# Kernel tuning notes

Measured on AMD Instinct MI355X. Metric: run time of the kernel, lower is better.

## Reference

```python
import jax, jax.numpy as jnp
import numpy as np

D_MODEL = 1024
NUM_HEADS = 16
HEAD_DIM = D_MODEL // NUM_HEADS


def setup_inputs() -> dict:
    key = jax.random.key(0)
    ks = jax.random.split(key, 9)
    B, S = 2, 2048
    s = 1.0 / np.sqrt(D_MODEL)
    return {
        "x": jax.random.normal(ks[0], (B, S, D_MODEL), dtype=jnp.float32),
        "Wq": jax.random.normal(ks[1], (D_MODEL, D_MODEL), dtype=jnp.float32) * s,
        "bq": jnp.zeros((D_MODEL,), dtype=jnp.float32),
        "Wk": jax.random.normal(ks[2], (D_MODEL, D_MODEL), dtype=jnp.float32) * s,
        "bk": jnp.zeros((D_MODEL,), dtype=jnp.float32),
        "Wv": jax.random.normal(ks[3], (D_MODEL, D_MODEL), dtype=jnp.float32) * s,
        "bv": jnp.zeros((D_MODEL,), dtype=jnp.float32),
        "Wo": jax.random.normal(ks[4], (D_MODEL, D_MODEL), dtype=jnp.float32) * s,
        "bo": jnp.zeros((D_MODEL,), dtype=jnp.float32),
    }


def reference(x, Wq, bq, Wk, bk, Wv, bv, Wo, bo):
    B, S, _ = x.shape
    # projections; weights stored as (in, out) so y = x @ W + b
    def heads(y):  # [B,S,D] -> [B,H,S,Dh]
        return y.reshape(B, S, NUM_HEADS, HEAD_DIM).transpose(0, 2, 1, 3)

    Q = heads(x @ Wq + bq)
    K = heads(x @ Wk + bk)
    V = heads(x @ Wv + bv)
    scale = 1.0 / np.sqrt(HEAD_DIM).astype(np.float32)
    scores = jnp.einsum("bhqd,bhkd->bhqk", Q, K) * scale  # [B,H,S,S]
    attn = jax.nn.softmax(scores, axis=-1)
    ctx = jnp.einsum("bhqk,bhkd->bhqd", attn, V)  # [B,H,S,Dh]
    ctx = ctx.transpose(0, 2, 1, 3).reshape(B, S, D_MODEL)
    return ctx @ Wo + bo
```

## Files before the change

### kernel.cpp

```cpp
#include <hip/hip_runtime.h>
#include <hip/hip_bf16.h>

#define SEQ   2048
#define NH    16
#define HD    64
#define DM    1024
#define MROWS 4096

#define QSCALE 0.125f
#define RTHR 5.545177444479562f

typedef __attribute__((ext_vector_type(4))) float f32x4;
typedef __attribute__((ext_vector_type(8))) short s16x8;
typedef __attribute__((ext_vector_type(4))) short s16x4;

__device__ __forceinline__ short f2bf(float f) {
  union { float f; unsigned u; } v; v.f = f;
  return (short)((v.u + 0x7fff + ((v.u >> 16) & 1)) >> 16);
}

__device__ __forceinline__ void gload_lds16(const short* g, short* l) {
  __builtin_amdgcn_global_load_lds(
      (const __attribute__((address_space(1))) void*)g,
      (__attribute__((address_space(3))) void*)l, 16, 0, 0);
}

#define SWZ(row, gg) ((((row) << 3) + (((gg) ^ ((row) & 7)))) << 3)

__global__ void cvt_x(const float* __restrict__ x, short* __restrict__ xb) {
  int i = (blockIdx.x * 256 + threadIdx.x) * 8;
  const float4* p = reinterpret_cast<const float4*>(x + i);
  float4 a = p[0], b = p[1];
  s16x8 o;
  o[0] = f2bf(a.x); o[1] = f2bf(a.y); o[2] = f2bf(a.z); o[3] = f2bf(a.w);
  o[4] = f2bf(b.x); o[5] = f2bf(b.y); o[6] = f2bf(b.z); o[7] = f2bf(b.w);
  *reinterpret_cast<s16x8*>(xb + i) = o;
}

__global__ void wtrans(const float* __restrict__ Wq, const float* __restrict__ Wk,
                       const float* __restrict__ Wv, const float* __restrict__ Wo,
                       short* __restrict__ WT) {
  __shared__ float tile[64][65];
  const float* W = (blockIdx.z == 0) ? Wq : (blockIdx.z == 1) ? Wk : (blockIdx.z == 2) ? Wv : Wo;
  short* dst = WT + (size_t)blockIdx.z * DM * DM;
  int kbase = blockIdx.x * 64;
  int nbase = blockIdx.y * 64;
  int t = threadIdx.x;
  {
    int n4 = (t & 15) * 4;
    #pragma unroll
    for (int rr = 0; rr < 4; ++rr) {
      int r = (t >> 4) + 16 * rr;
      float4 v = *reinterpret_cast<const float4*>(W + (size_t)(kbase + r) * DM + nbase + n4);
      tile[r][n4] = v.x; tile[r][n4 + 1] = v.y; tile[r][n4 + 2] = v.z; tile[r][n4 + 3] = v.w;
    }
  }
  __syncthreads();
  {
    int n = t >> 2, kc = (t & 3) * 16;
    short tmp[16];
    #pragma unroll
    for (int j = 0; j < 16; ++j) tmp[j] = f2bf(tile[kc + j][n]);
    s16x8* q = reinterpret_cast<s16x8*>(dst + (size_t)(nbase + n) * DM + kbase + kc);
    q[0] = *reinterpret_cast<s16x8*>(tmp);
    q[1] = *reinterpret_cast<s16x8*>(tmp + 8);
  }
}

__global__ __launch_bounds__(256, 2) void gemm_qkv(
    const short* __restrict__ A, const short* __restrict__ BT,
    const float* __restrict__ bias0, const float* __restrict__ bias1,
    const float* __restrict__ bias2,
    short* __restrict__ oQ, short* __restrict__ oK, short* __restrict__ oVt) {
  __shared__ __align__(16) short As[128 * 64];
  __shared__ __align__(16) short Bs[128 * 64];
  const int lin = blockIdx.x;
  const int wg = (lin & 7) * 96 + (lin >> 3);
  const int bx = wg & 31;
  const int by = wg >> 5;
  const int lane = threadIdx.x & 63;
  const int wid = threadIdx.x >> 6;
  const int q15 = lane & 15, g4 = lane >> 4;
  const int mbase = bx * 128;
  const int nbase = by * 128;
  const int wm = wid >> 1, wn = wid & 1;

  f32x4 acc[4][4] = {};
  const int srow = lane >> 3;
  const int sg = (lane & 7) ^ srow;

  for (int k0 = 0; k0 < DM; k0 += 64) {
    #pragma unroll
    for (int j = 0; j < 4; ++j) {
      int c = wid * 4 + j;
      int row = c * 8 + srow;
      gload_lds16(A + (size_t)(mbase + row) * DM + k0 + sg * 8, As + c * 512);
      gload_lds16(BT + (size_t)(nbase + row) * DM + k0 + sg * 8, Bs + c * 512);
    }
    __syncthreads();
    #pragma unroll
    for (int ks = 0; ks < 2; ++ks) {
      s16x8 af[4], bfr[4];
      #pragma unroll
      for (int m = 0; m < 4; ++m)
        af[m] = *reinterpret_cast<const s16x8*>(As + SWZ(wm * 64 + m * 16 + q15, ks * 4 + g4));
      #pragma unroll
      for (int n = 0; n < 4; ++n)
        bfr[n] = *reinterpret_cast<const s16x8*>(Bs + SWZ(wn * 64 + n * 16 + q15, ks * 4 + g4));
      #pragma unroll
      for (int m = 0; m < 4; ++m)
        #pragma unroll
        for (int n = 0; n < 4; ++n)
          acc[m][n] = __builtin_amdgcn_mfma_f32_16x16x32_bf16(af[m], bfr[n], acc[m][n], 0, 0, 0);
    }
    __syncthreads();
  }

  const int r0 = mbase + wm * 64;
  const int c0 = nbase + wn * 64;
  #pragma unroll
  for (int m = 0; m < 4; ++m) {
    #pragma unroll
    for (int n = 0; n < 4; ++n) {
      int rr = r0 + m * 16 + g4 * 4;
      int cc = c0 + n * 16 + q15;
      int seg = cc >> 10, c1 = cc & 1023;
      const float* bp = (seg == 0) ? bias0 : (seg == 1) ? bias1 : bias2;
      float bv = bp[c1];
      int h = c1 >> 6, d = c1 & 63;
      if (seg == 2) {
        s16x4 o;
        #pragma unroll
        for (int i = 0; i < 4; ++i) o[i] = f2bf(acc[m][n][i] + bv);
        int b = rr >> 11, s = rr & 2047;
        *reinterpret_cast<s16x4*>(
            oVt + ((size_t)(b * NH + h) * HD + d) * SEQ + s) = o;
      } else {
        short* dst = (seg == 0) ? oQ : oK;
        #pragma unroll
        for (int i = 0; i < 4; ++i) {
          int r = rr + i;
          float v = acc[m][n][i] + bv;
          if (seg == 0) v *= QSCALE;
          int b = r >> 11, s = r & 2047;
          size_t idx = (((size_t)(b * NH + h) * SEQ + s) << 6) + d;
          dst[idx] = f2bf(v);
        }
      }
    }
  }
}

__global__ __launch_bounds__(256, 2) void gemm_o(
    const short* __restrict__ A, const short* __restrict__ BT,
    const float* __restrict__ bias, float* __restrict__ oF) {
  __shared__ __align__(16) short As[64 * 64];
  __shared__ __align__(16) short Bs[128 * 64];
  const int lin = blockIdx.x;
  const int wg = (lin & 7) * 64 + (lin >> 3);
  const int bx = wg & 63;
  const int by = wg >> 6;
  const int lane = threadIdx.x & 63;
  const int wid = threadIdx.x >> 6;
  const int q15 = lane & 15, g4 = lane >> 4;
  const int mbase = bx * 64;
  const int nbase = by * 128;

  f32x4 acc[4][2] = {};
  const int srow = lane >> 3;
  const int sg = (lane & 7) ^ srow;

  for (int k0 = 0; k0 < DM; k0 += 64) {
    #pragma unroll
    for (int p = 0; p < 2; ++p)
      gload_lds16(A + (size_t)(mbase + p * 32 + wid * 8 + srow) * DM + k0 + sg * 8,
                  As + p * 2048 + wid * 512);
    #pragma unroll
    for (int p = 0; p < 4; ++p)
      gload_lds16(BT + (size_t)(nbase + p * 32 + wid * 8 + srow) * DM + k0 + sg * 8,
                  Bs + p * 2048 + wid * 512);
    __syncthreads();
    #pragma unroll
    for (int ks = 0; ks < 2; ++ks) {
      s16x8 af[4], bfr[2];
      #pragma unroll
      for (int m = 0; m < 4; ++m)
        af[m] = *reinterpret_cast<const s16x8*>(As + SWZ(m * 16 + q15, ks * 4 + g4));
      #pragma unroll
      for (int n = 0; n < 2; ++n)
        bfr[n] = *reinterpret_cast<const s16x8*>(Bs + SWZ(wid * 32 + n * 16 + q15, ks * 4 + g4));
      #pragma unroll
      for (int m = 0; m < 4; ++m)
        #pragma unroll
        for (int n = 0; n < 2; ++n)
          acc[m][n] = __builtin_amdgcn_mfma_f32_16x16x32_bf16(af[m], bfr[n], acc[m][n], 0, 0, 0);
    }
    __syncthreads();
  }

  #pragma unroll
  for (int m = 0; m < 4; ++m) {
    #pragma unroll
    for (int n = 0; n < 2; ++n) {
      int cc = nbase + wid * 32 + n * 16 + q15;
      float bv = bias[cc];
      #pragma unroll
      for (int i = 0; i < 4; ++i) {
        int r = mbase + m * 16 + g4 * 4 + i;
        oF[(size_t)r * DM + cc] = acc[m][n][i] + bv;
      }
    }
  }
}

__global__ __launch_bounds__(512, 4) void attn(const short* __restrict__ Q,
                                               const short* __restrict__ K,
                                               const short* __restrict__ Vt,
                                               short* __restrict__ ctx) {
  const int bh = blockIdx.y;
  const int lane = threadIdx.x & 63;
  const int wid = threadIdx.x >> 6;
  const int q15 = lane & 15, g4 = lane >> 4;
  const int qrow = blockIdx.x * 128 + wid * 16;
  const short* Qh = Q + (size_t)bh * SEQ * HD;
  const short* Kh = K + (size_t)bh * SEQ * HD;
  const short* Vh = Vt + (size_t)bh * HD * SEQ;

  __shared__ __align__(16) short Ks[2][64 * 64];
  __shared__ __align__(16) short Vs[2][64 * 64];
  __shared__ __align__(16) short Plds[8][16][72];
  short(*P)[72] = Plds[wid];

  const int t = threadIdx.x;
  const int srow = t >> 3;
  const int sg = (t & 7) ^ (srow & 7);
  const short* ksrc = Kh + (size_t)srow * HD + sg * 8;
  const short* vsrc = Vh + (size_t)srow * SEQ + sg * 8;

  s16x8 qf[2];
  #pragma unroll
  for (int ks = 0; ks < 2; ++ks)
    qf[ks] = *reinterpret_cast<const s16x8*>(
        Qh + (size_t)(qrow + q15) * HD + ks * 32 + g4 * 8);

  s16x8 ones;
  #pragma unroll
  for (int i = 0; i < 8; ++i) ones[i] = (short)0x3F80;

  f32x4 acco[4] = {};
  f32x4 lacc = {};
  float mrun = 0.f;

  gload_lds16(ksrc, Ks[0] + wid * 512);
  gload_lds16(vsrc, Vs[0] + wid * 512);
  __syncthreads();

  int cur = 0;
  for (int it = 0; it < SEQ / 64; ++it) {
    if (it + 1 < SEQ / 64) {
      gload_lds16(ksrc + (size_t)(it + 1) * 64 * HD, Ks[cur ^ 1] + wid * 512);
      gload_lds16(vsrc + (it + 1) * 64, Vs[cur ^ 1] + wid * 512);
    }
    const short* Kb = Ks[cur];
    const short* Vb = Vs[cur];

    f32x4 sacc[4] = {};
    #pragma unroll
    for (int kb = 0; kb < 4; ++kb) {
      s16x8 kf0 = *reinterpret_cast<const s16x8*>(Kb + SWZ(kb * 16 + q15, g4));
      s16x8 kf1 = *reinterpret_cast<const s16x8*>(Kb + SWZ(kb * 16 + q15, g4 + 4));
      sacc[kb] = __builtin_amdgcn_mfma_f32_16x16x32_bf16(kf0, qf[0], sacc[kb], 0, 0, 0);
      sacc[kb] = __builtin_amdgcn_mfma_f32_16x16x32_bf16(kf1, qf[1], sacc[kb], 0, 0, 0);
    }

    float t0 = fmaxf(fmaxf(sacc[0][0], sacc[0][1]), fmaxf(sacc[0][2], sacc[0][3]));
    float t1 = fmaxf(fmaxf(sacc[1][0], sacc[1][1]), fmaxf(sacc[1][2], sacc[1][3]));
    float t2 = fmaxf(fmaxf(sacc[2][0], sacc[2][1]), fmaxf(sacc[2][2], sacc[2][3]));
    float t3 = fmaxf(fmaxf(sacc[3][0], sacc[3][1]), fmaxf(sacc[3][2], sacc[3][3]));
    float tmax = fmaxf(fmaxf(t0, t1), fmaxf(t2, t3));

    if (it == 0) {
      float tm = fmaxf(tmax, __shfl_xor(tmax, 16));
      mrun = fmaxf(tm, __shfl_xor(tm, 32));
    }

    #pragma unroll
    for (int kb = 0; kb < 4; ++kb) {
      s16x4 pk;
      pk[0] = f2bf(__expf(sacc[kb][0] - mrun));
      pk[1] = f2bf(__expf(sacc[kb][1] - mrun));
      pk[2] = f2bf(__expf(sacc[kb][2] - mrun));
      pk[3] = f2bf(__expf(sacc[kb][3] - mrun));
      *reinterpret_cast<s16x4*>(&P[q15][kb * 16 + g4 * 4]) = pk;
    }
    s16x8 pf0 = *reinterpret_cast<const s16x8*>(&P[q15][g4 * 8]);
    s16x8 pf1 = *reinterpret_cast<const s16x8*>(&P[q15][32 + g4 * 8]);

    lacc = __builtin_amdgcn_mfma_f32_16x16x32_bf16(ones, pf0, lacc, 0, 0, 0);
    lacc = __builtin_amdgcn_mfma_f32_16x16x32_bf16(ones, pf1, lacc, 0, 0, 0);

    #pragma unroll
    for (int dvb = 0; dvb < 4; ++dvb) {
      s16x8 vf0 = *reinterpret_cast<const s16x8*>(Vb + SWZ(dvb * 16 + q15, g4));
      s16x8 vf1 = *reinterpret_cast<const s16x8*>(Vb + SWZ(dvb * 16 + q15, g4 + 4));
      acco[dvb] = __builtin_amdgcn_mfma_f32_16x16x32_bf16(vf0, pf0, acco[dvb], 0, 0, 0);
      acco[dvb] = __builtin_amdgcn_mfma_f32_16x16x32_bf16(vf1, pf1, acco[dvb], 0, 0, 0);
    }

    if (it > 0) {
      float tm = fmaxf(tmax, __shfl_xor(tmax, 16));
      tm = fmaxf(tm, __shfl_xor(tm, 32));
      if (!__all(tm <= mrun + RTHR)) {
        float mnew = fmaxf(mrun, tm);
        float r = __expf(mrun - mnew);
        lacc *= r;
        #pragma unroll
        for (int dvb = 0; dvb < 4; ++dvb) acco[dvb] *= r;
        mrun = mnew;
      }
    }

    __syncthreads();
    cur ^= 1;
  }

  const int b = bh >> 4, h = bh & 15;
  float inv = 1.f / lacc[0];
  int q = qrow + q15;
  #pragma unroll
  for (int dvb = 0; dvb < 4; ++dvb) {
    s16x4 o;
    #pragma unroll
    for (int i = 0; i < 4; ++i) o[i] = f2bf(acco[dvb][i] * inv);
    int d = dvb * 16 + g4 * 4;
    *reinterpret_cast<s16x4*>(ctx + ((size_t)b * SEQ + q) * DM + h * HD + d) = o;
  }
}

extern "C" void kernel_launch(void* const* d_in, const int* in_sizes, int n_in,
                              void* d_out, int out_size, void* d_ws, size_t ws_size,
                              hipStream_t stream) {
  const float* x = (const float*)d_in[0];
  const float* Wq = (const float*)d_in[1];
  const float* bq = (const float*)d_in[2];
  const float* Wk = (const float*)d_in[3];
  const float* bk = (const float*)d_in[4];
  const float* Wv = (const float*)d_in[5];
  const float* bv = (const float*)d_in[6];
  const float* Wo = (const float*)d_in[7];
  const float* bo = (const float*)d_in[8];

  char* ws = (char*)d_ws;
  const size_t MB8 = (size_t)8 << 20;
  short* xb  = (short*)(ws);
  short* WT  = (short*)(ws + 1 * MB8);
  short* Qb  = (short*)(ws + 2 * MB8);
  short* Kb  = (short*)(ws + 3 * MB8);
  short* Vtb = (short*)(ws + 5 * MB8);
  short* ctx = (short*)(ws + 6 * MB8);

  cvt_x<<<dim3(MROWS * DM / 2048), 256, 0, stream>>>(x, xb);
  wtrans<<<dim3(16, 16, 4), 256, 0, stream>>>(Wq, Wk, Wv, Wo, WT);
  gemm_qkv<<<dim3(768), 256, 0, stream>>>(xb, WT, bq, bk, bv, Qb, Kb, Vtb);
  attn<<<dim3(SEQ / 128, 32), 512, 0, stream>>>(Qb, Kb, Vtb, ctx);
  gemm_o<<<dim3(512), 256, 0, stream>>>(ctx, WT + (size_t)3072 * DM, bo, (float*)d_out);
}
```

Measured before the change: 135.8 us.

## Double-buffer LDS tiles in QKV and output projection GEMMs

Result: slower. 144.2 us (+6.2%).

```diff
diff --git a/kernel.cpp b/kernel.cpp
--- a/kernel.cpp
+++ b/kernel.cpp
@@ -72,8 +72,8 @@
     const float* __restrict__ bias0, const float* __restrict__ bias1,
     const float* __restrict__ bias2,
     short* __restrict__ oQ, short* __restrict__ oK, short* __restrict__ oVt) {
-  __shared__ __align__(16) short As[128 * 64];
-  __shared__ __align__(16) short Bs[128 * 64];
+  __shared__ __align__(16) short As[2][128 * 64];
+  __shared__ __align__(16) short Bs[2][128 * 64];
   const int lin = blockIdx.x;
   const int wg = (lin & 7) * 96 + (lin >> 3);
   const int bx = wg & 31;
@@ -89,24 +89,32 @@
   const int srow = lane >> 3;
   const int sg = (lane & 7) ^ srow;
 
-  for (int k0 = 0; k0 < DM; k0 += 64) {
+  auto stage = [&](int kt, int buf) {
+    const int k0 = kt * 64;
     #pragma unroll
     for (int j = 0; j < 4; ++j) {
       int c = wid * 4 + j;
       int row = c * 8 + srow;
-      gload_lds16(A + (size_t)(mbase + row) * DM + k0 + sg * 8, As + c * 512);
-      gload_lds16(BT + (size_t)(nbase + row) * DM + k0 + sg * 8, Bs + c * 512);
-    }
-    __syncthreads();
+      gload_lds16(A + (size_t)(mbase + row) * DM + k0 + sg * 8, As[buf] + c * 512);
+      gload_lds16(BT + (size_t)(nbase + row) * DM + k0 + sg * 8, Bs[buf] + c * 512);
+    }
+  };
+
+  stage(0, 0);
+  __syncthreads();
+
+  for (int kt = 0; kt < 16; ++kt) {
+    const int cur = kt & 1;
+    if (kt + 1 < 16) stage(kt + 1, cur ^ 1);
     #pragma unroll
     for (int ks = 0; ks < 2; ++ks) {
       s16x8 af[4], bfr[4];
       #pragma unroll
       for (int m = 0; m < 4; ++m)
-        af[m] = *reinterpret_cast<const s16x8*>(As + SWZ(wm * 64 + m * 16 + q15, ks * 4 + g4));
+        af[m] = *reinterpret_cast<const s16x8*>(As[cur] + SWZ(wm * 64 + m * 16 + q15, ks * 4 + g4));
       #pragma unroll
       for (int n = 0; n < 4; ++n)
-        bfr[n] = *reinterpret_cast<const s16x8*>(Bs + SWZ(wn * 64 + n * 16 + q15, ks * 4 + g4));
+        bfr[n] = *reinterpret_cast<const s16x8*>(Bs[cur] + SWZ(wn * 64 + n * 16 + q15, ks * 4 + g4));
       #pragma unroll
       for (int m = 0; m < 4; ++m)
         #pragma unroll
@@ -154,8 +162,8 @@
 __global__ __launch_bounds__(256, 2) void gemm_o(
     const short* __restrict__ A, const short* __restrict__ BT,
     const float* __restrict__ bias, float* __restrict__ oF) {
-  __shared__ __align__(16) short As[64 * 64];
-  __shared__ __align__(16) short Bs[128 * 64];
+  __shared__ __align__(16) short As[2][64 * 64];
+  __shared__ __align__(16) short Bs[2][128 * 64];
   const int lin = blockIdx.x;
   const int wg = (lin & 7) * 64 + (lin >> 3);
   const int bx = wg & 63;
@@ -170,25 +178,33 @@
   const int srow = lane >> 3;
   const int sg = (lane & 7) ^ srow;
 
-  for (int k0 = 0; k0 < DM; k0 += 64) {
+  auto stage = [&](int kt, int buf) {
+    const int k0 = kt * 64;
     #pragma unroll
     for (int p = 0; p < 2; ++p)
       gload_lds16(A + (size_t)(mbase + p * 32 + wid * 8 + srow) * DM + k0 + sg * 8,
-                  As + p * 2048 + wid * 512);
+                  As[buf] + p * 2048 + wid * 512);
     #pragma unroll
     for (int p = 0; p < 4; ++p)
       gload_lds16(BT + (size_t)(nbase + p * 32 + wid * 8 + srow) * DM + k0 + sg * 8,
-                  Bs + p * 2048 + wid * 512);
-    __syncthreads();
+                  Bs[buf] + p * 2048 + wid * 512);
+  };
+
+  stage(0, 0);
+  __syncthreads();
+
+  for (int kt = 0; kt < 16; ++kt) {
+    const int cur = kt & 1;
+    if (kt + 1 < 16) stage(kt + 1, cur ^ 1);
     #pragma unroll
     for (int ks = 0; ks < 2; ++ks) {
       s16x8 af[4], bfr[2];
       #pragma unroll
       for (int m = 0; m < 4; ++m)
-        af[m] = *reinterpret_cast<const s16x8*>(As + SWZ(m * 16 + q15, ks * 4 + g4));
+        af[m] = *reinterpret_cast<const s16x8*>(As[cur] + SWZ(m * 16 + q15, ks * 4 + g4));
       #pragma unroll
       for (int n = 0; n < 2; ++n)
-        bfr[n] = *reinterpret_cast<const s16x8*>(Bs + SWZ(wid * 32 + n * 16 + q15, ks * 4 + g4));
+        bfr[n] = *reinterpret_cast<const s16x8*>(Bs[cur] + SWZ(wid * 32 + n * 16 + q15, ks * 4 + g4));
       #pragma unroll
       for (int m = 0; m < 4; ++m)
         #pragma unroll
```
